# Performance work log

Measured on AMD Instinct MI355X. Metric: run time of the kernel, lower is better.

The kernel has to match this reference:

```python
import jax, jax.numpy as jnp
import numpy as np

N_NODES = 131072
N_EDGES = 4194304
H1, H2 = 16, 1


def setup_inputs() -> dict:
    key = jax.random.key(0)
    k = jax.random.split(key, 6)
    x = jax.random.uniform(k[0], (N_NODES, 2), dtype=jnp.float32)
    edge_index = jax.random.randint(k[1], (2, N_EDGES), 0, N_NODES, dtype=jnp.int64)
    # GCNConv weights (glorot-ish scale) and zero biases
    W1 = jax.random.normal(k[2], (2, H1), dtype=jnp.float32) * 0.5
    b1 = jnp.zeros((H1,), dtype=jnp.float32)
    W2 = jax.random.normal(k[3], (H1, H2), dtype=jnp.float32) * 0.25
    b2 = jnp.zeros((H2,), dtype=jnp.float32)
    return {"x": x, "W1": W1, "b1": b1, "W2": W2, "b2": b2, "edge_index": edge_index}


def gcn_layer(x, W, b, src, dst, n):
    # PyG GCNConv: h = D^{-1/2} (A+I) D^{-1/2} (x W) + b  (self-loops already in src/dst)
    h = x @ W                                              # [N, F_out]
    deg = jax.ops.segment_sum(jnp.ones(dst.shape[0], h.dtype), dst, num_segments=n)
    dinv = jax.lax.rsqrt(deg)                              # deg >= 1 thanks to self-loops
    norm = dinv[src] * dinv[dst]                           # [E+N]
    out = jax.ops.segment_sum(h[src] * norm[:, None], dst, num_segments=n)
    return out + b


def reference(x, W1, b1, W2, b2, edge_index):
    n = x.shape[0]
    loops = jnp.arange(n, dtype=edge_index.dtype)
    src = jnp.concatenate([edge_index[0], loops])          # add self-loops once
    dst = jnp.concatenate([edge_index[1], loops])
    h = jax.nn.relu(gcn_layer(x, W1, b1, src, dst, n))
    h = gcn_layer(h, W2, b2, src, dst, n)                  # [N, 1]
    scores = jax.nn.sigmoid(h)
    return scores[edge_index[0]]                           # gather per-edge source score [E, 1]
```

## Files before the change

### kernel.cpp

```cpp
#include <hip/hip_runtime.h>
#include <cmath>

typedef unsigned int uint;

constexpr int N  = 131072;
constexpr int E  = 4194304;
constexpr int F  = 16;
constexpr int NB = 512;
constexpr int NBLK  = 512;
constexpr int SCT   = 512;
constexpr int GT    = 1024;
constexpr int CHUNK = 8192;
constexpr int EPT   = 16;
constexpr int CAPB  = 9216;
constexpr int LT    = 1024;
constexpr uint SENT = 0xFFFFFFFFu;

constexpr float S1 = 4194304.0f;
constexpr float S2 = 65536.0f;

__global__ void __launch_bounds__(SCT) k_scatter(
        const int* __restrict__ src, const int* __restrict__ dst,
        uint* __restrict__ part, uint* __restrict__ dirw) {
    __shared__ uint h[NB];
    __shared__ uint wsum[8];
    __shared__ uint vals[CHUNK];
    int t = threadIdx.x, g = blockIdx.x;
    int lane = t & 63, w = t >> 6;
    h[t] = 0;
    __syncthreads();
    int d[EPT], s[EPT];
    const int4* src4 = (const int4*)src;
    const int4* dst4 = (const int4*)dst;
    int base4 = g * (CHUNK / 4);
#pragma unroll
    for (int k = 0; k < EPT / 4; ++k) {
        int4 d4 = dst4[base4 + k * SCT + t];
        int4 s4 = src4[base4 + k * SCT + t];
        d[4 * k + 0] = d4.x; d[4 * k + 1] = d4.y; d[4 * k + 2] = d4.z; d[4 * k + 3] = d4.w;
        s[4 * k + 0] = s4.x; s[4 * k + 1] = s4.y; s[4 * k + 2] = s4.z; s[4 * k + 3] = s4.w;
        atomicAdd(&h[d4.x >> 8], 1u);
        atomicAdd(&h[d4.y >> 8], 1u);
        atomicAdd(&h[d4.z >> 8], 1u);
        atomicAdd(&h[d4.w >> 8], 1u);
    }
    __syncthreads();
    uint v = h[t];
    uint sv = v;
#pragma unroll
    for (int off = 1; off < 64; off <<= 1) {
        uint n = __shfl_up(sv, off);
        if (lane >= off) sv += n;
    }
    if (lane == 63) wsum[w] = sv;
    __syncthreads();
    uint wo = 0;
    for (int i = 0; i < w; ++i) wo += wsum[i];
    sv += wo;
    uint ex = sv - v;
    dirw[(size_t)g * NB + t] = v | (ex << 16);
    __syncthreads();
    h[t] = ex;
    __syncthreads();
#pragma unroll
    for (int k = 0; k < EPT; ++k) {
        int b = d[k] >> 8;
        uint slot = atomicAdd(&h[b], 1u);
        vals[slot] = ((uint)s[k] << 8) | (uint)(d[k] & 255);
    }
    __syncthreads();
    uint4* part4 = (uint4*)(part + (size_t)g * CHUNK);
    const uint4* vals4 = (const uint4*)vals;
#pragma unroll
    for (int k = 0; k < EPT / 4; ++k)
        part4[k * SCT + t] = vals4[k * SCT + t];
}

__global__ void k_tr(const uint* __restrict__ in, uint* __restrict__ outm) {
    __shared__ uint tile[32][33];
    int bx = blockIdx.x, by = blockIdx.y;
    int tx = threadIdx.x, ty = threadIdx.y;
    tile[ty][tx] = in[(size_t)(by * 32 + ty) * NB + bx * 32 + tx];
    __syncthreads();
    outm[(size_t)(bx * 32 + ty) * NBLK + by * 32 + tx] = tile[tx][ty];
}

__global__ void __launch_bounds__(GT) k_gather(
        const uint* __restrict__ part, const uint* __restrict__ dirT,
        const float* __restrict__ x,
        uint* __restrict__ part2, uint* __restrict__ blen,
        float* __restrict__ dinv, float2* __restrict__ y) {
    __shared__ uint ps[NB + 1];
    __shared__ uint segoff[NB];
    __shared__ uint hw[16 * 256];
    __shared__ uint wsum[8];
    __shared__ uint stage[CAPB];
    int t = threadIdx.x, b = blockIdx.x;
    int lane = t & 63, w = t >> 6;
#pragma unroll
    for (int k = 0; k < 4; ++k) hw[k * GT + t] = 0;
    if (t < NB) {
        uint pd = dirT[(size_t)b * NBLK + t];
        uint len = pd & 0xFFFFu;
        segoff[t] = (uint)t * CHUNK + (pd >> 16);
        uint sv = len;
#pragma unroll
        for (int off = 1; off < 64; off <<= 1) {
            uint n = __shfl_up(sv, off);
            if (lane >= off) sv += n;
        }
        if (lane == 63) wsum[w] = sv;
        ps[t] = sv - len;
    }
    __syncthreads();
    if (t < NB) {
        uint wo = 0;
        for (int i = 0; i < w; ++i) wo += wsum[i];
        ps[t] += wo;
    }
    if (t == 0) {
        uint L = 0;
#pragma unroll
        for (int i = 0; i < 8; ++i) L += wsum[i];
        ps[NB] = L;
    }
    __syncthreads();
    uint L = ps[NB];
    for (uint i = t; i < L; i += GT) {
        uint lo = 0, hi = NB;
        while (hi - lo > 1) {
            uint mid = (lo + hi) >> 1;
            if (ps[mid] <= i) lo = mid; else hi = mid;
        }
        uint pk = part[segoff[lo] + (i - ps[lo])];
        if (i < (uint)CAPB) stage[i] = pk;
        atomicAdd(&hw[w * 256 + (pk & 255u)], 1u);
    }
    __syncthreads();
    uint Lc = (L > (uint)CAPB) ? (uint)CAPB : L;
    uint Lp = (Lc + 3u) & ~3u;
    uint* o2 = part2 + (size_t)b * CAPB;
    for (uint i = t; i < Lp; i += GT) o2[i] = (i < Lc) ? stage[i] : SENT;
    if (t == 0) blen[b] = Lp;
    if (t < 256) {
        uint c = 0;
#pragma unroll
        for (int k = 0; k < 16; ++k) c += hw[k * 256 + t];
        int node = (b << 8) + t;
        float di = rsqrtf(1.0f + (float)c);
        dinv[node] = di;
        float2 xv = ((const float2*)x)[node];
        y[node] = make_float2(di * xv.x, di * xv.y);
    }
}

__global__ void __launch_bounds__(LT) k_l1(
        const uint* __restrict__ part2, const uint* __restrict__ blen,
        const float2* __restrict__ y, const float* __restrict__ dinv,
        const float* __restrict__ W1, const float* __restrict__ b1,
        const float* __restrict__ W2, float* __restrict__ g2) {
    __shared__ int a0[16 * 256], a1[16 * 256];
    int t = threadIdx.x, b = blockIdx.x, w = t >> 6;
#pragma unroll
    for (int k = 0; k < 4; ++k) { a0[k * LT + t] = 0; a1[k * LT + t] = 0; }
    __syncthreads();
    uint L4 = blen[b] >> 2;
    const uint4* p4 = (const uint4*)(part2 + (size_t)b * CAPB);
    for (uint i = t; i < L4; i += LT) {
        uint4 q = p4[i];
        uint pk;
#pragma unroll
        for (int k = 0; k < 4; ++k) {
            pk = (k == 0) ? q.x : (k == 1) ? q.y : (k == 2) ? q.z : q.w;
            if (pk != SENT) {
                float2 ys = y[pk >> 8];
                atomicAdd(&a0[w * 256 + (pk & 255u)], __float2int_rn(ys.x * S1));
                atomicAdd(&a1[w * 256 + (pk & 255u)], __float2int_rn(ys.y * S1));
            }
        }
    }
    __syncthreads();
    if (t < 256) {
        int s0 = 0, s1 = 0;
#pragma unroll
        for (int k = 0; k < 16; ++k) { s0 += a0[k * 256 + t]; s1 += a1[k * 256 + t]; }
        int node = (b << 8) + t;
        float di = dinv[node];
        float2 yn = y[node];
        float A0 = di * ((float)s0 * (1.0f / S1) + yn.x);
        float A1 = di * ((float)s1 * (1.0f / S1) + yn.y);
        float acc = 0.0f;
#pragma unroll
        for (int f = 0; f < F; ++f) {
            float v = fmaf(A0, W1[f], fmaf(A1, W1[F + f], b1[f]));
            acc = fmaf(fmaxf(v, 0.0f), W2[f], acc);
        }
        g2[node] = di * acc;
    }
}

__global__ void __launch_bounds__(LT) k_l2(
        const uint* __restrict__ part2, const uint* __restrict__ blen,
        const float* __restrict__ g2, const float* __restrict__ dinv,
        const float* __restrict__ b2, float* __restrict__ scores) {
    __shared__ int a[16 * 256];
    int t = threadIdx.x, b = blockIdx.x, w = t >> 6;
#pragma unroll
    for (int k = 0; k < 4; ++k) a[k * LT + t] = 0;
    __syncthreads();
    uint L4 = blen[b] >> 2;
    const uint4* p4 = (const uint4*)(part2 + (size_t)b * CAPB);
    for (uint i = t; i < L4; i += LT) {
        uint4 q = p4[i];
        uint pk;
#pragma unroll
        for (int k = 0; k < 4; ++k) {
            pk = (k == 0) ? q.x : (k == 1) ? q.y : (k == 2) ? q.z : q.w;
            if (pk != SENT)
                atomicAdd(&a[w * 256 + (pk & 255u)], __float2int_rn(g2[pk >> 8] * S2));
        }
    }
    __syncthreads();
    if (t < 256) {
        int s = 0;
#pragma unroll
        for (int k = 0; k < 16; ++k) s += a[k * 256 + t];
        int node = (b << 8) + t;
        float acc = (float)s * (1.0f / S2);
        float v = fmaf(dinv[node], acc + g2[node], b2[0]);
        scores[node] = 1.0f / (1.0f + expf(-v));
    }
}

__global__ void k_out(const int* __restrict__ src, const float* __restrict__ scores,
                      float* __restrict__ out) {
    int i = blockIdx.x * blockDim.x + threadIdx.x;
    if (i >= E / 4) return;
    int4 s4 = ((const int4*)src)[i];
    float4 o;
    o.x = scores[s4.x];
    o.y = scores[s4.y];
    o.z = scores[s4.z];
    o.w = scores[s4.w];
    ((float4*)out)[i] = o;
}

extern "C" void kernel_launch(void* const* d_in, const int* in_sizes, int n_in,
                              void* d_out, int out_size, void* d_ws, size_t ws_size,
                              hipStream_t stream) {
    const float* x  = (const float*)d_in[0];
    const float* W1 = (const float*)d_in[1];
    const float* b1 = (const float*)d_in[2];
    const float* W2 = (const float*)d_in[3];
    const float* b2 = (const float*)d_in[4];
    const int*   ei = (const int*)d_in[5];
    const int* src = ei;
    const int* dst = ei + E;

    uint* dirw    = (uint*)d_ws;
    uint* dirT    = dirw + (size_t)NBLK * NB;
    uint* blen    = dirT + (size_t)NBLK * NB;
    float* dinv   = (float*)(blen + NB);
    float2* y     = (float2*)(dinv + N);
    float* g2     = (float*)(y + N);
    float* scores = g2 + N;
    uint* part2   = (uint*)(scores + N);

    uint* part  = (uint*)d_out;
    float* out  = (float*)d_out;

    k_scatter<<<NBLK,              SCT,           0, stream>>>(src, dst, part, dirw);
    k_tr     <<<dim3(16, 16),      dim3(32, 32),  0, stream>>>(dirw, dirT);
    k_gather <<<NB,                GT,            0, stream>>>(part, dirT, x, part2,
                                                               blen, dinv, y);
    k_l1     <<<NB,                LT,            0, stream>>>(part2, blen, y, dinv,
                                                               W1, b1, W2, g2);
    k_l2     <<<NB,                LT,            0, stream>>>(part2, blen, g2, dinv,
                                                               b2, scores);
    k_out    <<<E / 4 / 256,       256,           0, stream>>>(src, scores, out);
}
```

Before: 168.8 us.

## Drop transpose kernel, gather segments per 16-lane group, batch y loads in l1

Removes the separate directory transpose kernel; the gather kernel now reads the directory column-wise with strided loads instead. The gather loop no longer binary-searches a prefix sum per element. Each 16-lane subgroup walks one source segment directly and writes straight to part2, with no LDS staging buffer, and only the padding slots are filled with sentinels. In k_l1 the four y loads per uint4 are issued before the atomics, to expose memory-level parallelism. The cost is strided directory reads, possible lane imbalance across segments of different lengths, and less coalesced part2 writes.

```diff
diff --git a/kernel.cpp b/kernel.cpp
--- a/kernel.cpp
+++ b/kernel.cpp
@@ -76,17 +76,8 @@
         part4[k * SCT + t] = vals4[k * SCT + t];
 }
 
-__global__ void k_tr(const uint* __restrict__ in, uint* __restrict__ outm) {
-    __shared__ uint tile[32][33];
-    int bx = blockIdx.x, by = blockIdx.y;
-    int tx = threadIdx.x, ty = threadIdx.y;
-    tile[ty][tx] = in[(size_t)(by * 32 + ty) * NB + bx * 32 + tx];
-    __syncthreads();
-    outm[(size_t)(bx * 32 + ty) * NBLK + by * 32 + tx] = tile[tx][ty];
-}
-
 __global__ void __launch_bounds__(GT) k_gather(
-        const uint* __restrict__ part, const uint* __restrict__ dirT,
+        const uint* __restrict__ part, const uint* __restrict__ dirw,
         const float* __restrict__ x,
         uint* __restrict__ part2, uint* __restrict__ blen,
         float* __restrict__ dinv, float2* __restrict__ y) {
@@ -94,13 +85,12 @@
     __shared__ uint segoff[NB];
     __shared__ uint hw[16 * 256];
     __shared__ uint wsum[8];
-    __shared__ uint stage[CAPB];
     int t = threadIdx.x, b = blockIdx.x;
     int lane = t & 63, w = t >> 6;
 #pragma unroll
     for (int k = 0; k < 4; ++k) hw[k * GT + t] = 0;
     if (t < NB) {
-        uint pd = dirT[(size_t)b * NBLK + t];
+        uint pd = dirw[(size_t)t * NB + b];
         uint len = pd & 0xFFFFu;
         segoff[t] = (uint)t * CHUNK + (pd >> 16);
         uint sv = len;
@@ -119,28 +109,30 @@
         ps[t] += wo;
     }
     if (t == 0) {
-        uint L = 0;
-#pragma unroll
-        for (int i = 0; i < 8; ++i) L += wsum[i];
-        ps[NB] = L;
+        uint Lt = 0;
+#pragma unroll
+        for (int i = 0; i < 8; ++i) Lt += wsum[i];
+        ps[NB] = Lt;
     }
     __syncthreads();
     uint L = ps[NB];
-    for (uint i = t; i < L; i += GT) {
-        uint lo = 0, hi = NB;
-        while (hi - lo > 1) {
-            uint mid = (lo + hi) >> 1;
-            if (ps[mid] <= i) lo = mid; else hi = mid;
-        }
-        uint pk = part[segoff[lo] + (i - ps[lo])];
-        if (i < (uint)CAPB) stage[i] = pk;
-        atomicAdd(&hw[w * 256 + (pk & 255u)], 1u);
+    uint* o2 = part2 + (size_t)b * CAPB;
+    int sub = lane >> 4, l16 = lane & 15;
+#pragma unroll
+    for (int pass = 0; pass < 8; ++pass) {
+        int r = pass * 64 + w * 4 + sub;
+        uint off = segoff[r], base = ps[r], len = ps[r + 1] - base;
+        for (uint j = l16; j < len; j += 16) {
+            uint pk = part[off + j];
+            atomicAdd(&hw[w * 256 + (pk & 255u)], 1u);
+            if (base + j < (uint)CAPB) o2[base + j] = pk;
+        }
     }
     __syncthreads();
     uint Lc = (L > (uint)CAPB) ? (uint)CAPB : L;
     uint Lp = (Lc + 3u) & ~3u;
-    uint* o2 = part2 + (size_t)b * CAPB;
-    for (uint i = t; i < Lp; i += GT) o2[i] = (i < Lc) ? stage[i] : SENT;
+    uint i2 = Lc + (uint)t;
+    if (i2 < Lp) o2[i2] = SENT;
     if (t == 0) blen[b] = Lp;
     if (t < 256) {
         uint c = 0;
@@ -168,16 +160,20 @@
     const uint4* p4 = (const uint4*)(part2 + (size_t)b * CAPB);
     for (uint i = t; i < L4; i += LT) {
         uint4 q = p4[i];
-        uint pk;
-#pragma unroll
-        for (int k = 0; k < 4; ++k) {
-            pk = (k == 0) ? q.x : (k == 1) ? q.y : (k == 2) ? q.z : q.w;
-            if (pk != SENT) {
-                float2 ys = y[pk >> 8];
-                atomicAdd(&a0[w * 256 + (pk & 255u)], __float2int_rn(ys.x * S1));
-                atomicAdd(&a1[w * 256 + (pk & 255u)], __float2int_rn(ys.y * S1));
-            }
-        }
+        bool v0 = q.x != SENT, v1 = q.y != SENT, v2 = q.z != SENT, v3 = q.w != SENT;
+        float2 y0, y1, y2, y3;
+        if (v0) y0 = y[q.x >> 8];
+        if (v1) y1 = y[q.y >> 8];
+        if (v2) y2 = y[q.z >> 8];
+        if (v3) y3 = y[q.w >> 8];
+        if (v0) { atomicAdd(&a0[w * 256 + (q.x & 255u)], __float2int_rn(y0.x * S1));
+                  atomicAdd(&a1[w * 256 + (q.x & 255u)], __float2int_rn(y0.y * S1)); }
+        if (v1) { atomicAdd(&a0[w * 256 + (q.y & 255u)], __float2int_rn(y1.x * S1));
+                  atomicAdd(&a1[w * 256 + (q.y & 255u)], __float2int_rn(y1.y * S1)); }
+        if (v2) { atomicAdd(&a0[w * 256 + (q.z & 255u)], __float2int_rn(y2.x * S1));
+                  atomicAdd(&a1[w * 256 + (q.z & 255u)], __float2int_rn(y2.y * S1)); }
+        if (v3) { atomicAdd(&a0[w * 256 + (q.w & 255u)], __float2int_rn(y3.x * S1));
+                  atomicAdd(&a1[w * 256 + (q.w & 255u)], __float2int_rn(y3.y * S1)); }
     }
     __syncthreads();
     if (t < 256) {
@@ -258,8 +254,7 @@
     const int* dst = ei + E;
 
     uint* dirw    = (uint*)d_ws;
-    uint* dirT    = dirw + (size_t)NBLK * NB;
-    uint* blen    = dirT + (size_t)NBLK * NB;
+    uint* blen    = dirw + (size_t)NBLK * NB;
     float* dinv   = (float*)(blen + NB);
     float2* y     = (float2*)(dinv + N);
     float* g2     = (float*)(y + N);
@@ -269,13 +264,9 @@
     uint* part  = (uint*)d_out;
     float* out  = (float*)d_out;
 
-    k_scatter<<<NBLK,              SCT,           0, stream>>>(src, dst, part, dirw);
-    k_tr     <<<dim3(16, 16),      dim3(32, 32),  0, stream>>>(dirw, dirT);
-    k_gather <<<NB,                GT,            0, stream>>>(part, dirT, x, part2,
-                                                               blen, dinv, y);
-    k_l1     <<<NB,                LT,            0, stream>>>(part2, blen, y, dinv,
-                                                               W1, b1, W2, g2);
-    k_l2     <<<NB,                LT,            0, stream>>>(part2, blen, g2, dinv,
-                                                               b2, scores);
-    k_out    <<<E / 4 / 256,       256,           0, stream>>>(src, scores, out);
-}
+    k_scatter<<<NBLK,        SCT, 0, stream>>>(src, dst, part, dirw);
+    k_gather <<<NB,          GT,  0, stream>>>(part, dirw, x, part2, blen, dinv, y);
+    k_l1     <<<NB,          LT,  0, stream>>>(part2, blen, y, dinv, W1, b1, W2, g2);
+    k_l2     <<<NB,          LT,  0, stream>>>(part2, blen, g2, dinv, b2, scores);
+    k_out    <<<E / 4 / 256, 256, 0, stream>>>(src, scores, out);
+}
```

Result: faster. 164.8 us (median of 2 runs) (-2.3%).
